# Optimization experiments

Hardware: AMD Instinct MI355X
Metric: run time of the kernel (lower is better)

## Reference

```python
import jax, jax.numpy as jnp
import numpy as np

B, T, LMAX = 8, 4000, 2048
VOCAB, D, H = 20000, 128, 128
SCALE = float(H) ** 0.5  # torch uses pow(hidden_dim, 0.5) with hidden_dim=128 even though feature dim is 256


def setup_inputs() -> dict:
    key = jax.random.key(0)
    ks = jax.random.split(key, 22)
    def n(k, sh, s=0.05):
        return jax.random.normal(k, sh, dtype=jnp.float32) * s
    token_ids = jax.random.randint(ks[0], (B, T), 0, VOCAB)
    lens = jax.random.randint(ks[1], (B,), LMAX // 4, LMAX).at[0].set(LMAX)
    return dict(
        token_ids=token_ids, lens=lens,
        embed=n(ks[2], (VOCAB, D)),
        gru_wih0=n(ks[3], (2, 3 * H, D)), gru_whh0=n(ks[4], (2, 3 * H, H)),
        gru_bih0=n(ks[5], (2, 3 * H)), gru_bhh0=n(ks[6], (2, 3 * H)),
        gru_wih1=n(ks[7], (2, 3 * H, 2 * H)), gru_whh1=n(ks[8], (2, 3 * H, H)),
        gru_bih1=n(ks[9], (2, 3 * H)), gru_bhh1=n(ks[10], (2, 3 * H)),
        conv_w=n(ks[11], (3, D, D, 2)), conv_b=n(ks[12], (3, D)),
        Wa_w=n(ks[13], (2 * H, 4 * H)), Wa_b=n(ks[14], (2 * H,)),
        VT_w=n(ks[15], (1, 2 * H)), VT_b=n(ks[16], (1,)),
        Qw=n(ks[17], (2 * H, 2 * H)), Kw=n(ks[18], (2 * H, 2 * H)), Vw=n(ks[19], (2 * H, 2 * H)),
        fc_w=n(ks[20], (6, 2 * H)), fc_b=n(ks[21], (6,)),
    )


def _gru_dir(x, mask, Wih, Whh, bih, bhh):
    # One direction of a torch GRU layer with packed-sequence semantics:
    # outputs are zero past each sample's length; state frozen there.
    xg = jnp.einsum('bld,gd->blg', x, Wih) + bih   # [B, L, 3H] precomputed input gates
    xg = jnp.swapaxes(xg, 0, 1)                    # [L, B, 3H]
    m = jnp.swapaxes(mask, 0, 1)                   # [L, B]
    h0 = jnp.zeros((x.shape[0], H), x.dtype)

    def step(h, inp):
        g, mt = inp
        hh = h @ Whh.T + bhh
        r = jax.nn.sigmoid(g[:, :H] + hh[:, :H])
        z = jax.nn.sigmoid(g[:, H:2 * H] + hh[:, H:2 * H])
        nn_ = jnp.tanh(g[:, 2 * H:] + r * hh[:, 2 * H:])
        hn = (1.0 - z) * nn_ + z * h
        h2 = jnp.where(mt[:, None] > 0, hn, h)
        return h2, hn * mt[:, None]

    _, out = jax.lax.scan(step, h0, (xg, m))
    return jnp.swapaxes(out, 0, 1)                 # [B, L, H]


def _bi_gru_layer(x, mask, rev_idx, wih, whh, bih, bhh):
    out_f = _gru_dir(x, mask, wih[0], whh[0], bih[0], bhh[0])
    # packed bi-GRU: backward direction runs over each sample's reversed VALID segment
    xr = jnp.take_along_axis(x, rev_idx[:, :, None], axis=1)
    out_b = _gru_dir(xr, mask, wih[1], whh[1], bih[1], bhh[1])
    out_b = jnp.take_along_axis(out_b, rev_idx[:, :, None], axis=1) * mask[:, :, None]
    return jnp.concatenate([out_f, out_b], axis=-1)


def _additive_attn(s, enc, mask, Wa_w, Wa_b, VT_w, VT_b):
    sb = jnp.broadcast_to(s, enc.shape)
    x = jnp.concatenate([sb, enc], axis=-1)                     # [B, L, 4H]
    sh = jnp.tanh(jnp.einsum('blk,hk->blh', x, Wa_w) + Wa_b)
    res = jnp.einsum('blh,oh->blo', sh, VT_w)[..., 0] + VT_b[0]  # [B, L]
    # torch multiplies scores by 0/1 mask BEFORE softmax (pads get score 0, not -inf)
    w = jax.nn.softmax(res * mask, axis=-1)
    return jnp.sum(enc * w[..., None], axis=1, keepdims=True)   # [B, 1, 2H]


def _forward(embed, gru_wih0, gru_whh0, gru_bih0, gru_bhh0, gru_wih1, gru_whh1, gru_bih1, gru_bhh1,
             conv_w, conv_b, Wa_w, Wa_b, VT_w, VT_b, Qw, Kw, Vw, fc_w, fc_b, token_ids, lens):
    emb = embed[token_ids]                                      # [B, T, D]
    tpos = jnp.arange(LMAX)
    mask = (tpos[None, :] < lens[:, None]).astype(emb.dtype)    # [B, LMAX]
    rev_idx = jnp.where(tpos[None, :] < lens[:, None], lens[:, None] - 1 - tpos[None, :], tpos[None, :])
    pad_data = emb[:, :LMAX] * mask[..., None]                  # pad_packed_sequence zeroes pads

    # conv backbone runs on the FULL 4000-length padded embedding (as in torch), then trimmed/masked
    x = jnp.swapaxes(emb, 1, 2)                                 # [B, D, T]
    for i in range(3):
        x = jax.lax.conv_general_dilated(x, conv_w[i], (1,), 'VALID',
                                         dimension_numbers=('NCH', 'OIH', 'NCH'))
        x = jax.nn.relu(x + conv_b[i][None, :, None])
    conv_out = jnp.swapaxes(x, 1, 2)[:, :LMAX] * mask[..., None]  # [B, LMAX, D]

    h1 = _bi_gru_layer(pad_data, mask, rev_idx, gru_wih0, gru_whh0, gru_bih0, gru_bhh0)
    enc = _bi_gru_layer(h1, mask, rev_idx, gru_wih1, gru_whh1, gru_bih1, gru_bhh1)  # [B, LMAX, 2H]

    tmean = jnp.mean(conv_out, axis=1)                          # mean over padded length, as torch
    s = jnp.repeat(tmean, 2, axis=-1)[:, None, :]               # expand+reshape => interleaved duplicate [B,1,2H]

    inp2 = jnp.concatenate([pad_data, pad_data], axis=-1)       # [B, LMAX, 2H]
    Q = inp2 @ Qw.T
    K = inp2 @ Kw.T
    V = inp2 @ Vw.T
    scores = jnp.einsum('bqd,bkd->bqk', Q, K) / SCALE
    W = jax.nn.softmax(scores, axis=0)                          # torch F.softmax implicit dim -> 0 for 3D input
    W = W * mask[:, :, None]                                    # mask broadcast over key axis (query rows masked)
    Z = jnp.einsum('bqk,bkd->bqd', W, V)
    sa = jnp.sum(Z, axis=1, keepdims=True)                      # [B, 1, 2H]

    d1 = _additive_attn(s, enc, mask, Wa_w, Wa_b, VT_w, VT_b)
    d2 = _additive_attn(sa, enc, mask, Wa_w, Wa_b, VT_w, VT_b)
    dinput = 0.5 * (d1 + d2)                                    # mean over the concat dim
    return dinput @ fc_w.T + fc_b                               # [B, 1, 6]


def reference(token_ids, lens, embed, gru_wih0, gru_whh0, gru_bih0, gru_bhh0, gru_wih1, gru_whh1,
              gru_bih1, gru_bhh1, conv_w, conv_b, Wa_w, Wa_b, VT_w, VT_b, Qw, Kw, Vw, fc_w, fc_b):
    return _forward(embed, gru_wih0, gru_whh0, gru_bih0, gru_bhh0, gru_wih1, gru_whh1, gru_bih1,
                    gru_bhh1, conv_w, conv_b, Wa_w, Wa_b, VT_w, VT_b, Qw, Kw, Vw, fc_w, fc_b,
                    token_ids, lens)
```

## Files before the change

kernel.cpp:

```cpp
#include <hip/hip_runtime.h>
#include <stdint.h>

typedef unsigned short u16;
typedef unsigned int u32;
typedef __attribute__((ext_vector_type(8))) short short8;
typedef __attribute__((ext_vector_type(8))) u16 u16x8;
typedef __attribute__((ext_vector_type(4))) float f32x4;
typedef __attribute__((ext_vector_type(2))) float f32x2;
typedef __attribute__((ext_vector_type(2))) u32 u32x2;

#define DEVINL static __device__ __forceinline__

#if !__has_builtin(__builtin_amdgcn_exp2f)
#define __builtin_amdgcn_exp2f(x) exp2f(x)
#endif
#if !__has_builtin(__builtin_amdgcn_rcpf)
#define __builtin_amdgcn_rcpf(x) (1.0f/(x))
#endif

#define MFMA16(a, b, c) __builtin_amdgcn_mfma_f32_16x16x32_bf16((a), (b), (c), 0, 0, 0)

constexpr float LOG2E_C    = 1.4426950408889634f;
constexpr float TWOLOG2E_C = 2.8853900817779268f;
constexpr float RSCALE_LG  = 1.4426950408889634f / 11.313708498984761f;

constexpr size_t A256(size_t x){ return (x + 255) & ~(size_t)255; }
constexpr size_t OFS_EMB   = 0;
constexpr size_t OFS_PAD   = A256(OFS_EMB  + (size_t)8*2051*128*2);
constexpr size_t OFS_X1    = A256(OFS_PAD  + (size_t)8*2048*128*2);
constexpr size_t OFS_X2    = A256(OFS_X1   + (size_t)8*2050*128*2);
constexpr size_t OFS_QKVW  = A256(OFS_X2   + (size_t)8*2049*128*2);
constexpr size_t OFS_WA2   = A256(OFS_QKVW + (size_t)3*256*128*2);
constexpr size_t OFS_CONVW = A256(OFS_WA2  + (size_t)256*256*2);
constexpr size_t OFS_WIH0  = A256(OFS_CONVW+ (size_t)3*128*256*2);
constexpr size_t OFS_WIH1  = A256(OFS_WIH0 + (size_t)2*384*128*2);
constexpr size_t OFS_BIASX = A256(OFS_WIH1 + (size_t)2*384*256*2);
constexpr size_t OFS_BHHN  = A256(OFS_BIASX+ (size_t)2*2*384*4);
constexpr size_t OFS_Q     = A256(OFS_BHHN + (size_t)2*2*128*4);
constexpr size_t OFS_K     = A256(OFS_Q    + (size_t)8*2048*256*2);
constexpr size_t OFS_V     = A256(OFS_K    + (size_t)8*2048*256*2);
constexpr size_t OFS_CS    = A256(OFS_V    + (size_t)8*2048*256*2);
constexpr size_t OFS_TM    = A256(OFS_CS   + (size_t)8*2048*4);
constexpr size_t OFS_XG    = A256(OFS_TM   + (size_t)8*128*4);
constexpr size_t OFS_H1    = A256(OFS_XG   + (size_t)2*2048*8*384*4);
constexpr size_t OFS_ENC   = A256(OFS_H1   + (size_t)8*2048*256*2);
constexpr size_t OFS_ENCW  = A256(OFS_ENC  + (size_t)8*2048*256*2);
constexpr size_t OFS_SA    = A256(OFS_ENCW + (size_t)8*2048*256*4);
constexpr size_t OFS_RES   = A256(OFS_SA   + (size_t)8*256*4);
constexpr size_t OFS_DV    = A256(OFS_RES  + (size_t)8*2*2048*4);

DEVINL u16 f2bf(float f){
  u32 u = __builtin_bit_cast(u32, f);
  u32 r = (u + 0x7FFFu + ((u >> 16) & 1u)) >> 16;
  return (u16)r;
}
DEVINL float bf2f(u16 s){ return __builtin_bit_cast(float, (u32)s << 16); }

DEVINL short8 ld8cvt(const float* p, float sc){
  short8 o;
#pragma unroll
  for (int e = 0; e < 8; ++e) o[e] = (short)f2bf(p[e]*sc);
  return o;
}

DEVINL u32 cvtpk(float lo, float hi){
  u32 r;
  asm("v_cvt_pk_bf16_f32 %0, %1, %2" : "=v"(r) : "v"(lo), "v"(hi));
  return r;
}

DEVINL float sel4(const f32x4 v, int rr){
  float a = (rr & 1) ? v[1] : v[0];
  float bq = (rr & 1) ? v[3] : v[2];
  return (rr & 2) ? bq : a;
}

__global__ __launch_bounds__(256) void k_prep(
    const int* tok, const int* lens, const float* embed,
    const float* wih0, const float* wih1,
    const float* bih0, const float* bhh0, const float* bih1, const float* bhh1,
    const float* convw, const float* WaW, const float* Qw, const float* Kw, const float* Vw,
    char* ws)
{
  u16* emb_bf   = (u16*)(ws + OFS_EMB);
  u16* pad_bf   = (u16*)(ws + OFS_PAD);
  u16* qkvw     = (u16*)(ws + OFS_QKVW);
  u16* wa2      = (u16*)(ws + OFS_WA2);
  u16* convw_bf = (u16*)(ws + OFS_CONVW);
  u16* wih0_bf  = (u16*)(ws + OFS_WIH0);
  u16* wih1_bf  = (u16*)(ws + OFS_WIH1);
  float* biasx  = (float*)(ws + OFS_BIASX);
  float* bhhn   = (float*)(ws + OFS_BHHN);
  float* colsum = (float*)(ws + OFS_CS);
  float* tmean  = (float*)(ws + OFS_TM);
  const int S0 = 8*2051*128, S1 = 8*2048*128, S2 = 3*256*128, S3 = 256*256, S4 = 3*128*256;
  const int S5 = 2*384*128, S6 = 2*384*256, S7 = 2*2*384 + 2*2*128, S8 = 8*2048 + 8*128;
  const int TOT = S0+S1+S2+S3+S4+S5+S6+S7+S8;
  for (int i = blockIdx.x*256 + threadIdx.x; i < TOT; i += gridDim.x*256){
    int j = i;
    if (j < S0){
      int b = j / (2051*128); int r = j - b*(2051*128); int t = r >> 7, dd = r & 127;
      emb_bf[j] = f2bf(embed[(size_t)tok[b*4000 + t]*128 + dd]);
      continue;
    }
    j -= S0;
    if (j < S1){
      int b = j >> 18; int r = j & 262143; int t = r >> 7, dd = r & 127;
      float v = (t < lens[b]) ? embed[(size_t)tok[b*4000 + t]*128 + dd] : 0.f;
      pad_bf[j] = f2bf(v); continue;
    }
    j -= S1;
    if (j < S2){
      int z = j >> 15; int r = j & 32767; int o = r >> 7, k2 = r & 127;
      const float* W = (z == 0) ? Qw : (z == 1) ? Kw : Vw;
      qkvw[j] = f2bf(W[o*256 + k2] + W[o*256 + 128 + k2]); continue;
    }
    j -= S2;
    if (j < S3){ int h = j >> 8, k2 = j & 255; wa2[j] = f2bf(WaW[(size_t)h*512 + 256 + k2]); continue; }
    j -= S3;
    if (j < S4){
      int ly = j >> 15; int r = j & 32767; int o = r >> 8, k2 = r & 255;
      int i2 = k2 & 127, kap = k2 >> 7;
      convw_bf[j] = f2bf(convw[((size_t)(ly*128 + o)*128 + i2)*2 + kap]); continue;
    }
    j -= S4;
    if (j < S5){ wih0_bf[j] = f2bf(wih0[j]); continue; }
    j -= S5;
    if (j < S6){ wih1_bf[j] = f2bf(wih1[j]); continue; }
    j -= S6;
    if (j < S7){
      if (j < 1536){
        int ly = j / 768; int r = j - ly*768; int d = r / 384, g = r % 384;
        float bi = (ly ? bih1 : bih0)[d*384 + g];
        float bh = (ly ? bhh1 : bhh0)[d*384 + g];
        biasx[j] = (g < 256) ? (-LOG2E_C*(bi + bh)) : (TWOLOG2E_C*bi);
      } else {
        int j2 = j - 1536; int ly = j2 >> 8; int r = j2 & 255; int d = r >> 7, jj = r & 127;
        bhhn[j2] = TWOLOG2E_C*((ly ? bhh1 : bhh0)[d*384 + 256 + jj]);
      }
      continue;
    }
    j -= S7;
    if (j < 8*2048) colsum[j] = 0.f; else tmean[j - 8*2048] = 0.f;
  }
}

template<int KIN>
__global__ __launch_bounds__(256, 1) void k_xg(const int* lens, char* ws){
  const int tt = blockIdx.x, b = blockIdx.y, dir = blockIdx.z;
  constexpr int LAYER = (KIN == 128) ? 0 : 1;
  const u16* in = (KIN == 128) ? (const u16*)(ws + OFS_PAD) : (const u16*)(ws + OFS_H1);
  const u16* wmat = ((KIN == 128) ? (const u16*)(ws + OFS_WIH0) : (const u16*)(ws + OFS_WIH1))
                    + (size_t)dir*384*KIN;
  const float* biasx = (const float*)(ws + OFS_BIASX) + (LAYER*2 + dir)*384;
  float* xg = (float*)(ws + OFS_XG) + (size_t)dir*2048*3072;
  const int lenb = lens[b];
  __shared__ __align__(16) u16 sA[64][KIN + 8];
  constexpr int CH = KIN/8;
  const int tid = threadIdx.x, w = tid >> 6, l = tid & 63, rowg = l >> 4, cl = l & 15;
  for (int idx = tid; idx < 64*CH; idx += 256){
    int row = idx / CH, chn = idx % CH;
    int t = tt*64 + row;
    int tr = dir ? ((t < lenb) ? (lenb - 1 - t) : t) : t;
    *(u16x8*)&sA[row][chn*8] = *(const u16x8*)(in + ((size_t)(b*2048 + tr))*KIN + chn*8);
  }
  __syncthreads();
  f32x4 acc[24];
#pragma unroll
  for (int nt = 0; nt < 24; ++nt) acc[nt] = f32x4{0.f,0.f,0.f,0.f};
#pragma unroll
  for (int kk = 0; kk < KIN/32; ++kk){
    short8 a = *(const short8*)&sA[w*16 + cl][kk*32 + rowg*8];
#pragma unroll
    for (int nt = 0; nt < 24; ++nt){
      short8 bb = *(const short8*)(wmat + (size_t)(nt*16 + cl)*KIN + kk*32 + rowg*8);
      acc[nt] = MFMA16(a, bb, acc[nt]);
    }
  }
#pragma unroll
  for (int nt = 0; nt < 24; ++nt){
    const int g = nt*16 + cl;
    const float bx = biasx[g];
    const float sc = (nt < 16) ? -LOG2E_C : TWOLOG2E_C;
#pragma unroll
    for (int r = 0; r < 4; ++r){
      const int t = tt*64 + w*16 + rowg*4 + r;
      xg[((size_t)t*8 + b)*384 + g] = sc*acc[nt][r] + bx;
    }
  }
}

DEVINL void rec_block(char* smem, const float* xg_all, const float* whh_all,
    const float* bhhn_all, const int* lens, u16* out, int dir, int b)
{
  const float* xg  = xg_all + (size_t)dir*2048*3072 + b*384;
  const float* whh = whh_all + (size_t)dir*384*128;
  const float* bnd = bhhn_all + dir*128;
  const int tid = threadIdx.x;
  const int u = tid >> 6, l = tid & 63;
  const int c = l & 15, q = l >> 4;
  const int rsel = c & 3;
  const int j = u*16 + q*4 + rsel;
  const bool writer = (c < 4);
  const bool dirb = (dir != 0);
  const int lenb = lens[b];

  u16 (*hbuf)[128] = (u16(*)[128])smem;
  if (tid < 256) (&hbuf[0][0])[tid] = 0;

  short8 aR[4], aZ[4], aN[4];
#pragma unroll
  for (int kk = 0; kk < 4; ++kk){
    int k0 = kk*32 + q*8;
    int row = u*16 + c;
    aR[kk] = ld8cvt(whh + (size_t)(row)*128 + k0, -LOG2E_C);
    aZ[kk] = ld8cvt(whh + (size_t)(128 + row)*128 + k0, -LOG2E_C);
    aN[kk] = ld8cvt(whh + (size_t)(256 + row)*128 + k0, TWOLOG2E_C);
  }
  f32x4 bnU;
#pragma unroll
  for (int r = 0; r < 4; ++r) bnU[r] = bnd[u*16 + q*4 + r];

  const int offR = u*16 + q*4;
  const int offXN = 256 + j;
  u16* outp = out + (size_t)b*2048*256 + dir*128 + j;
  float hp = 0.f;

#define LOAD_STAGE(T_, Rv, Zv, Xn) do {              \
    const float* pb_ = xg + (size_t)(T_)*3072;       \
    Rv = *(const f32x4*)(pb_ + offR);                \
    Zv = *(const f32x4*)(pb_ + offR + 128);          \
    Xn = pb_[offXN];                                 \
  } while (0)

#define REC_STEP(T_, PF_, CUR_, Rv, Zv, Xn) do {                                      \
    short8 bf0_ = *(const short8*)(&hbuf[CUR_][0] + (q*8 + 0*32));                    \
    short8 bf1_ = *(const short8*)(&hbuf[CUR_][0] + (q*8 + 1*32));                    \
    short8 bf2_ = *(const short8*)(&hbuf[CUR_][0] + (q*8 + 2*32));                    \
    short8 bf3_ = *(const short8*)(&hbuf[CUR_][0] + (q*8 + 3*32));                    \
    f32x4 cR_ = MFMA16(aR[0], bf0_, Rv);                                              \
    f32x4 cZ_ = MFMA16(aZ[0], bf0_, Zv);                                              \
    f32x4 cN_ = MFMA16(aN[0], bf0_, bnU);                                             \
    const float* pfb_ = xg + (size_t)(PF_)*3072;                                      \
    Rv = *(const f32x4*)(pfb_ + offR);                                                \
    Zv = *(const f32x4*)(pfb_ + offR + 128);                                          \
    float Xnew_ = pfb_[offXN];                                                        \
    cR_ = MFMA16(aR[1], bf1_, cR_);                                                   \
    cZ_ = MFMA16(aZ[1], bf1_, cZ_);                                                   \
    cN_ = MFMA16(aN[1], bf1_, cN_);                                                   \
    cR_ = MFMA16(aR[2], bf2_, cR_);                                                   \
    cZ_ = MFMA16(aZ[2], bf2_, cZ_);                                                   \
    cN_ = MFMA16(aN[2], bf2_, cN_);                                                   \
    cR_ = MFMA16(aR[3], bf3_, cR_);                                                   \
    cZ_ = MFMA16(aZ[3], bf3_, cZ_);                                                   \
    cN_ = MFMA16(aN[3], bf3_, cN_);                                                   \
    const bool v_ = (T_) < lenb;                                                      \
    float gR = sel4(cR_, rsel);                                                       \
    float gZ = sel4(cZ_, rsel);                                                       \
    float gN = sel4(cN_, rsel);                                                       \
    float Rg = __builtin_amdgcn_rcpf(1.f + __builtin_amdgcn_exp2f(gR));               \
    float Zg = __builtin_amdgcn_rcpf(1.f + __builtin_amdgcn_exp2f(gZ));               \
    float y  = Xn + Rg*gN;                                                            \
    float NN = 1.f - 2.f*__builtin_amdgcn_rcpf(1.f + __builtin_amdgcn_exp2f(y));      \
    float hn = NN + Zg*(hp - NN);                                                     \
    hp = hn;                                                                          \
    Xn = Xnew_;                                                                       \
    u32 pk_ = cvtpk(hn, hn);                                                          \
    if (writer){                                                                      \
      hbuf[(CUR_) ^ 1][j] = (u16)pk_;                                                 \
      int to_ = dirb ? (v_ ? (lenb - 1 - (T_)) : (T_)) : (T_);                        \
      outp[(size_t)to_*256] = v_ ? (u16)pk_ : (u16)0;                                 \
    }                                                                                 \
    asm volatile("s_waitcnt lgkmcnt(0)" ::: "memory");                                \
    __builtin_amdgcn_s_barrier();                                                     \
  } while (0)

  f32x4 R0v, Z0v; float X0;
  f32x4 R1v, Z1v; float X1;
  f32x4 R2v, Z2v; float X2;
  f32x4 R3v, Z3v; float X3;
  __syncthreads();
  LOAD_STAGE(0, R0v, Z0v, X0);
  LOAD_STAGE(1, R1v, Z1v, X1);
  LOAD_STAGE(2, R2v, Z2v, X2);
  LOAD_STAGE(3, R3v, Z3v, X3);
  for (int t = 0; t < 2048; t += 4){
    int p4 = (t + 4 < 2048) ? (t + 4) : 2047;
    int p5 = (t + 5 < 2048) ? (t + 5) : 2047;
    int p6 = (t + 6 < 2048) ? (t + 6) : 2047;
    int p7 = (t + 7 < 2048) ? (t + 7) : 2047;
    REC_STEP(t + 0, p4, 0, R0v, Z0v, X0);
    REC_STEP(t + 1, p5, 1, R1v, Z1v, X1);
    REC_STEP(t + 2, p6, 0, R2v, Z2v, X2);
    REC_STEP(t + 3, p7, 1, R3v, Z3v, X3);
  }
#undef LOAD_STAGE
#undef REC_STEP
}

DEVINL void qkv_role(char* smem, char* ws, int tt, int b, int z){
  const u16* in = (const u16*)(ws + OFS_PAD);
  const u16* wmat = (const u16*)(ws + OFS_QKVW) + (size_t)z*256*128;
  u16* out = (u16*)(ws + ((z == 0) ? OFS_Q : (z == 1) ? OFS_K : OFS_V));
  u16 (*sA)[136] = (u16(*)[136])smem;
  const int tid = threadIdx.x;
  if (tid < 256){
    for (int idx = tid; idx < 64*16; idx += 256){
      int row = idx >> 4, chn = idx & 15;
      int t = tt*64 + row;
      *(u16x8*)&sA[row][chn*8] = *(const u16x8*)(in + ((size_t)(b*2048 + t))*128 + chn*8);
    }
  }
  __syncthreads();
  if (tid < 256){
    const int w = tid >> 6, l = tid & 63, rowg = l >> 4, cl = l & 15;
    f32x4 acc[16];
#pragma unroll
    for (int nt = 0; nt < 16; ++nt) acc[nt] = f32x4{0.f,0.f,0.f,0.f};
#pragma unroll
    for (int kk = 0; kk < 4; ++kk){
      short8 a = *(const short8*)&sA[w*16 + cl][kk*32 + rowg*8];
#pragma unroll
      for (int nt = 0; nt < 16; ++nt){
        short8 bb = *(const short8*)(wmat + (size_t)(nt*16 + cl)*128 + kk*32 + rowg*8);
        acc[nt] = MFMA16(a, bb, acc[nt]);
      }
    }
#pragma unroll
    for (int nt = 0; nt < 16; ++nt){
      int o = nt*16 + cl;
#pragma unroll
      for (int r = 0; r < 4; ++r){
        int t = tt*64 + w*16 + rowg*4 + r;
        out[((size_t)(b*2048 + t))*256 + o] = f2bf(acc[nt][r]);
      }
    }
  }
}

DEVINL void conv_layer_pass(u16 (*bi)[136], u16 (*bo)[136], const u16* wm, const float* bias,
                            int OUT_R, int w, int rowg, int cl){
#pragma unroll
  for (int pass = 0; pass < 2; ++pass){
    if (pass == 1 && !(w == 0 && OUT_R > 64)) break;
    const int rt = (pass == 0) ? w : 4;
    f32x4 acc[8];
#pragma unroll
    for (int nt = 0; nt < 8; ++nt) acc[nt] = f32x4{0.f,0.f,0.f,0.f};
#pragma unroll
    for (int kk = 0; kk < 8; ++kk){
      const int rofs = (kk >= 4) ? 1 : 0;
      short8 a = *(const short8*)&bi[rt*16 + cl + rofs][(kk & 3)*32 + rowg*8];
#pragma unroll
      for (int nt = 0; nt < 8; ++nt){
        short8 bb = *(const short8*)(wm + (size_t)(nt*16 + cl)*256 + kk*32 + rowg*8);
        acc[nt] = MFMA16(a, bb, acc[nt]);
      }
    }
#pragma unroll
    for (int nt = 0; nt < 8; ++nt){
      int o = nt*16 + cl;
      float bv = bias[o];
#pragma unroll
      for (int r = 0; r < 4; ++r){
        int ro = rt*16 + rowg*4 + r;
        if (ro < OUT_R) bo[ro][o] = f2bf(fmaxf(acc[nt][r] + bv, 0.f));
      }
    }
  }
}

DEVINL void conv_role(char* smem, const int* lens, const float* convb, char* ws, int tt, int b){
  const u16* emb = (const u16*)(ws + OFS_EMB);
  const u16* cw  = (const u16*)(ws + OFS_CONVW);
  float* tmean = (float*)(ws + OFS_TM);
  u16 (*bufA)[136] = (u16(*)[136])smem;
  u16 (*bufB)[136] = (u16(*)[136])(smem + 82*136*2);
  const int tid = threadIdx.x;
  const int w = tid >> 6, l = tid & 63, rowg = l >> 4, cl = l & 15;
  if (tid < 256){
    for (int idx = tid; idx < 67*16; idx += 256){
      int row = idx >> 4, chn = idx & 15;
      *(u16x8*)&bufA[row][chn*8] = *(const u16x8*)(emb + ((size_t)(b*2051 + tt*64 + row))*128 + chn*8);
    }
  }
  __syncthreads();
  if (tid < 256) conv_layer_pass(bufA, bufB, cw + (size_t)0*128*256, convb + 0,   66, w, rowg, cl);
  __syncthreads();
  if (tid < 256) conv_layer_pass(bufB, bufA, cw + (size_t)1*128*256, convb + 128, 65, w, rowg, cl);
  __syncthreads();
  if (tid < 256){
    const int lenb = lens[b];
    const u16* wm = cw + (size_t)2*128*256;
    f32x4 acc[8];
#pragma unroll
    for (int nt = 0; nt < 8; ++nt) acc[nt] = f32x4{0.f,0.f,0.f,0.f};
#pragma unroll
    for (int kk = 0; kk < 8; ++kk){
      const int rofs = (kk >= 4) ? 1 : 0;
      short8 a = *(const short8*)&bufA[w*16 + cl + rofs][(kk & 3)*32 + rowg*8];
#pragma unroll
      for (int nt = 0; nt < 8; ++nt){
        short8 bb = *(const short8*)(wm + (size_t)(nt*16 + cl)*256 + kk*32 + rowg*8);
        acc[nt] = MFMA16(a, bb, acc[nt]);
      }
    }
#pragma unroll
    for (int nt = 0; nt < 8; ++nt){
      int o = nt*16 + cl;
      float bias = convb[2*128 + o];
      float s = 0.f;
#pragma unroll
      for (int r = 0; r < 4; ++r){
        int t = tt*64 + w*16 + rowg*4 + r;
        if (t < lenb) s += fmaxf(acc[nt][r] + bias, 0.f);
      }
      s += __shfl_xor(s, 16); s += __shfl_xor(s, 32);
      if (l < 16) atomicAdd(&tmean[b*128 + o], s);
    }
  }
}

DEVINL void scores_role(char* smem, const int* lens, char* ws, int kt, int qt){
  const u16* Qp = (const u16*)(ws + OFS_Q);
  const u16* Kp = (const u16*)(ws + OFS_K);
  float* colsum = (float*)(ws + OFS_CS);
  u16 (*sQ)[264] = (u16(*)[264])smem;
  u16 (*sK)[264] = (u16(*)[264])(smem + 64*264*2);
  float (*cbuf)[64] = (float(*)[64])(smem + 2*64*264*2);
  const int tid = threadIdx.x, w = tid >> 6, l = tid & 63, rowg = l >> 4, cl = l & 15;
  if (tid < 256)
    for (int i = tid; i < 512; i += 256) cbuf[i >> 6][i & 63] = 0.f;
  f32x4 c[8][4];
#pragma unroll
  for (int b = 0; b < 8; ++b)
#pragma unroll
    for (int nt = 0; nt < 4; ++nt) c[b][nt] = f32x4{0.f,0.f,0.f,0.f};
#pragma unroll
  for (int b = 0; b < 8; ++b){
    __syncthreads();
    if (tid < 256){
      for (int idx = tid; idx < 4096; idx += 256){
        int which = idx >> 11, row = (idx >> 5) & 63, ch = idx & 31;
        if (which){
          *(u16x8*)&sK[row][ch*8] = *(const u16x8*)(Kp + ((size_t)(b*2048 + kt*64 + row))*256 + ch*8);
        } else {
          *(u16x8*)&sQ[row][ch*8] = *(const u16x8*)(Qp + ((size_t)(b*2048 + qt*64 + row))*256 + ch*8);
        }
      }
    }
    __syncthreads();
    if (tid < 256){
#pragma unroll
      for (int kk = 0; kk < 8; ++kk){
        short8 a = *(const short8*)&sQ[w*16 + cl][kk*32 + rowg*8];
#pragma unroll
        for (int nt = 0; nt < 4; ++nt){
          short8 bb = *(const short8*)&sK[nt*16 + cl][kk*32 + rowg*8];
          c[b][nt] = MFMA16(a, bb, c[b][nt]);
        }
      }
    }
  }
  if (tid < 256){
    int lenv[8];
#pragma unroll
    for (int b = 0; b < 8; ++b) lenv[b] = lens[b];
    const int q0 = qt*64 + w*16 + rowg*4;
    float cs[8][4];
#pragma unroll
    for (int b = 0; b < 8; ++b)
#pragma unroll
      for (int nt = 0; nt < 4; ++nt) cs[b][nt] = 0.f;
#pragma unroll
    for (int nt = 0; nt < 4; ++nt){
#pragma unroll
      for (int r = 0; r < 4; ++r){
        float m = c[0][nt][r];
#pragma unroll
        for (int b = 1; b < 8; ++b) m = fmaxf(m, c[b][nt][r]);
        float e[8], s = 0.f;
#pragma unroll
        for (int b = 0; b < 8; ++b){ e[b] = __builtin_amdgcn_exp2f((c[b][nt][r] - m)*RSCALE_LG); s += e[b]; }
        float ri = __builtin_amdgcn_rcpf(s);
#pragma unroll
        for (int b = 0; b < 8; ++b)
          if (q0 + r < lenv[b]) cs[b][nt] += e[b]*ri;
      }
    }
#pragma unroll
    for (int b = 0; b < 8; ++b)
#pragma unroll
      for (int nt = 0; nt < 4; ++nt){
        float v = cs[b][nt];
        v += __shfl_xor(v, 16); v += __shfl_xor(v, 32);
        if (l < 16) atomicAdd(&cbuf[b][nt*16 + l], v);
      }
  }
  __syncthreads();
  if (tid < 256){
    for (int i = tid; i < 512; i += 256)
      atomicAdd(&colsum[(size_t)(i >> 6)*2048 + kt*64 + (i & 63)], cbuf[i >> 6][i & 63]);
  }
}

__global__ __launch_bounds__(512, 2) void k_fusedA(const int* lens, const float* convb, char* ws,
    const float* whh0, u16* outH1)
{
  __shared__ __align__(16) char smem[90112];
  const int bid = blockIdx.x;
  if (bid < 16){
    rec_block(smem, (const float*)(ws + OFS_XG), whh0, (const float*)(ws + OFS_BHHN),
              lens, outH1, bid >> 3, bid & 7);
    return;
  }
  int r = bid - 16;
  if (r < 768){
    int z = r >> 8, rem = r & 255, b = rem >> 5, tt = rem & 31;
    qkv_role(smem, ws, tt, b, z);
    return;
  }
  r -= 768;
  conv_role(smem, lens, convb, ws, r & 31, r >> 5);
}

__global__ __launch_bounds__(512, 2) void k_fusedB(const int* lens, char* ws,
    const float* whh1, u16* outENC)
{
  __shared__ __align__(16) char smem[90112];
  const int bid = blockIdx.x;
  if (bid < 16){
    rec_block(smem, (const float*)(ws + OFS_XG), whh1, (const float*)(ws + OFS_BHHN) + 2*128,
              lens, outENC, bid >> 3, bid & 7);
    return;
  }
  int r = bid - 16;
  scores_role(smem, lens, ws, r & 31, r >> 5);
}

__global__ __launch_bounds__(256, 1) void k_encw(char* ws){
  const int tt = blockIdx.x, b = blockIdx.y;
  const u16* in = (const u16*)(ws + OFS_ENC);
  const u16* wmat = (const u16*)(ws + OFS_WA2);
  float* out = (float*)(ws + OFS_ENCW);
  __shared__ __align__(16) u16 sA[64][264];
  const int tid = threadIdx.x, w = tid >> 6, l = tid & 63, rowg = l >> 4, cl = l & 15;
  for (int idx = tid; idx < 64*32; idx += 256){
    int row = idx >> 5, chn = idx & 31;
    int t = tt*64 + row;
    *(u16x8*)&sA[row][chn*8] = *(const u16x8*)(in + ((size_t)(b*2048 + t))*256 + chn*8);
  }
  __syncthreads();
  f32x4 acc[16];
#pragma unroll
  for (int nt = 0; nt < 16; ++nt) acc[nt] = f32x4{0.f,0.f,0.f,0.f};
#pragma unroll
  for (int kk = 0; kk < 8; ++kk){
    short8 a = *(const short8*)&sA[w*16 + cl][kk*32 + rowg*8];
#pragma unroll
    for (int nt = 0; nt < 16; ++nt){
      short8 bb = *(const short8*)(wmat + (size_t)(nt*16 + cl)*256 + kk*32 + rowg*8);
      acc[nt] = MFMA16(a, bb, acc[nt]);
    }
  }
#pragma unroll
  for (int nt = 0; nt < 16; ++nt){
    int h = nt*16 + cl;
#pragma unroll
    for (int r = 0; r < 4; ++r){
      int t = tt*64 + w*16 + rowg*4 + r;
      out[((size_t)(b*2048 + t))*256 + h] = acc[nt][r];
    }
  }
}

__global__ __launch_bounds__(256) void k_sa(char* ws){
  const int b = blockIdx.x, d = threadIdx.x;
  const float* cs = (const float*)(ws + OFS_CS) + (size_t)b*2048;
  const u16* V = (const u16*)(ws + OFS_V) + (size_t)b*2048*256;
  float a0 = 0.f, a1 = 0.f, a2 = 0.f, a3 = 0.f;
  for (int k = 0; k < 2048; k += 4){
    a0 += cs[k + 0]*bf2f(V[(size_t)(k + 0)*256 + d]);
    a1 += cs[k + 1]*bf2f(V[(size_t)(k + 1)*256 + d]);
    a2 += cs[k + 2]*bf2f(V[(size_t)(k + 2)*256 + d]);
    a3 += cs[k + 3]*bf2f(V[(size_t)(k + 3)*256 + d]);
  }
  ((float*)(ws + OFS_SA))[b*256 + d] = (a0 + a1) + (a2 + a3);
}

__global__ __launch_bounds__(256) void k_res(const int* lens, const float* WaW, const float* Wab,
    const float* VTw, const float* VTb, char* ws){
  const int b = blockIdx.x, x = blockIdx.y, chb = blockIdx.z;
  const float* tm = (const float*)(ws + OFS_TM) + b*128;
  const float* sa = (const float*)(ws + OFS_SA) + b*256;
  const float* encW = (const float*)(ws + OFS_ENCW);
  float* res = (float*)(ws + OFS_RES) + ((size_t)b*2 + x)*2048;
  __shared__ float sw[256];
  __shared__ float vt[256];
  const int tid = threadIdx.x;
  {
    int h = tid;
    float acc = Wab[h];
    if (x == 0){
      for (int j = 0; j < 128; ++j)
        acc += tm[j]*(1.f/2048.f)*(WaW[(size_t)h*512 + 2*j] + WaW[(size_t)h*512 + 2*j + 1]);
    } else {
      for (int k = 0; k < 256; ++k) acc += sa[k]*WaW[(size_t)h*512 + k];
    }
    sw[h] = acc;
    vt[h] = VTw[h];
  }
  __syncthreads();
  const int lenb = lens[b];
  const int lsub = tid >> 2, q = tid & 3;
  const float vtb = VTb[0];
#pragma unroll
  for (int pass = 0; pass < 4; ++pass){
    const int ll = chb*256 + pass*64 + lsub;
    const float* er = encW + ((size_t)(b*2048 + ll))*256 + q*64;
    float racc = 0.f;
    for (int j = 0; j < 64; ++j){
      float u = er[j] + sw[q*64 + j];
      float th = 1.f - 2.f*__builtin_amdgcn_rcpf(1.f + __builtin_amdgcn_exp2f(u*TWOLOG2E_C));
      racc += th*vt[q*64 + j];
    }
    racc += __shfl_xor(racc, 1);
    racc += __shfl_xor(racc, 2);
    if (q == 0) res[ll] = (ll < lenb) ? (racc + vtb) : 0.f;
  }
}

__global__ __launch_bounds__(256) void k_attnfin(char* ws){
  const int b = blockIdx.x, x = blockIdx.y;
  const float* res = (const float*)(ws + OFS_RES) + ((size_t)b*2 + x)*2048;
  const u16* enc = (const u16*)(ws + OFS_ENC);
  float* dvec = (float*)(ws + OFS_DV);
  __shared__ float sv[2048];
  __shared__ float red[8];
  const int tid = threadIdx.x;
  float m = -3.0e38f;
  for (int i = tid; i < 2048; i += 256){ float v = res[i]; sv[i] = v; m = fmaxf(m, v); }
#pragma unroll
  for (int o = 1; o < 64; o <<= 1) m = fmaxf(m, __shfl_xor(m, o));
  if ((tid & 63) == 0) red[tid >> 6] = m;
  __syncthreads();
  m = fmaxf(fmaxf(red[0], red[1]), fmaxf(red[2], red[3]));
  __syncthreads();
  float s = 0.f;
  for (int i = tid; i < 2048; i += 256){ float e = __builtin_amdgcn_exp2f((sv[i] - m)*LOG2E_C); sv[i] = e; s += e; }
#pragma unroll
  for (int o = 1; o < 64; o <<= 1) s += __shfl_xor(s, o);
  if ((tid & 63) == 0) red[tid >> 6] = s;
  __syncthreads();
  const float S = red[0] + red[1] + red[2] + red[3];
  const float ri = 1.0f/S;
  const int h = tid;
  float a0 = 0.f, a1 = 0.f, a2 = 0.f, a3 = 0.f;
  for (int l0 = 0; l0 < 2048; l0 += 4){
    a0 += sv[l0 + 0]*bf2f(enc[((size_t)(b*2048 + l0 + 0))*256 + h]);
    a1 += sv[l0 + 1]*bf2f(enc[((size_t)(b*2048 + l0 + 1))*256 + h]);
    a2 += sv[l0 + 2]*bf2f(enc[((size_t)(b*2048 + l0 + 2))*256 + h]);
    a3 += sv[l0 + 3]*bf2f(enc[((size_t)(b*2048 + l0 + 3))*256 + h]);
  }
  dvec[((size_t)b*2 + x)*256 + h] = ((a0 + a1) + (a2 + a3))*ri;
}

__global__ __launch_bounds__(64) void k_final(const float* fcw, const float* fcb, char* ws, float* outp){
  const int i = threadIdx.x;
  if (i >= 48) return;
  const int b = i/6, o = i%6;
  const float* dv = (const float*)(ws + OFS_DV);
  float acc = fcb[o];
  for (int h = 0; h < 256; ++h)
    acc += 0.5f*(dv[((size_t)b*2 + 0)*256 + h] + dv[((size_t)b*2 + 1)*256 + h])*fcw[o*256 + h];
  outp[i] = acc;
}

extern "C" void kernel_launch(void* const* d_in, const int* in_sizes, int n_in,
                              void* d_out, int out_size, void* d_ws, size_t ws_size,
                              hipStream_t stream)
{
  const int* tok    = (const int*)d_in[0];
  const int* lens   = (const int*)d_in[1];
  const float* embed= (const float*)d_in[2];
  const float* wih0 = (const float*)d_in[3];
  const float* whh0 = (const float*)d_in[4];
  const float* bih0 = (const float*)d_in[5];
  const float* bhh0 = (const float*)d_in[6];
  const float* wih1 = (const float*)d_in[7];
  const float* whh1 = (const float*)d_in[8];
  const float* bih1 = (const float*)d_in[9];
  const float* bhh1 = (const float*)d_in[10];
  const float* convw= (const float*)d_in[11];
  const float* convb= (const float*)d_in[12];
  const float* WaW  = (const float*)d_in[13];
  const float* Wab  = (const float*)d_in[14];
  const float* VTw  = (const float*)d_in[15];
  const float* VTb  = (const float*)d_in[16];
  const float* Qw   = (const float*)d_in[17];
  const float* Kw   = (const float*)d_in[18];
  const float* Vw   = (const float*)d_in[19];
  const float* fcw  = (const float*)d_in[20];
  const float* fcb  = (const float*)d_in[21];
  char* ws = (char*)d_ws;
  float* outp = (float*)d_out;

  hipLaunchKernelGGL(k_prep, dim3(2048), dim3(256), 0, stream,
      tok, lens, embed, wih0, wih1, bih0, bhh0, bih1, bhh1, convw, WaW, Qw, Kw, Vw, ws);
  hipLaunchKernelGGL((k_xg<128>), dim3(32,8,2), dim3(256), 0, stream, lens, ws);
  hipLaunchKernelGGL(k_fusedA, dim3(16 + 768 + 256), dim3(512), 0, stream,
      lens, convb, ws, whh0, (u16*)(ws + OFS_H1));
  hipLaunchKernelGGL((k_xg<256>), dim3(32,8,2), dim3(256), 0, stream, lens, ws);
  hipLaunchKernelGGL(k_fusedB, dim3(16 + 1024), dim3(512), 0, stream,
      lens, ws, whh1, (u16*)(ws + OFS_ENC));
  hipLaunchKernelGGL(k_sa, dim3(8), dim3(256), 0, stream, ws);
  hipLaunchKernelGGL(k_encw, dim3(32,8), dim3(256), 0, stream, ws);
  hipLaunchKernelGGL(k_res, dim3(8,2,8), dim3(256), 0, stream, lens, WaW, Wab, VTw, VTb, ws);
  hipLaunchKernelGGL(k_attnfin, dim3(8,2), dim3(256), 0, stream, ws);
  hipLaunchKernelGGL(k_final, dim3(1), dim3(64), 0, stream, fcw, fcb, ws, outp);
  (void)in_sizes; (void)n_in; (void)out_size; (void)ws_size;
}
```

Measured before the change: 1.799 ms.

## Merge tail kernels, split attention reduction, raise MFMA priority in recurrence

Merges k_encw and k_sa into a single launch (k_tail1) that branches on block index. It also splits k_attnfin's 2048-step reduction across 4 z-blocks that combine partial sums with atomicAdd into a dvec buffer now zeroed in k_prep. The GRU recurrence wraps its MFMA chain in s_setprio(1)/s_setprio(0) to favor the latency-critical wave. The aim is to cut launch overhead and serial tail latency; the cost is redundant softmax work per chunk and non-deterministic float accumulation order.

```diff
diff --git a/kernel.cpp b/kernel.cpp
--- a/kernel.cpp
+++ b/kernel.cpp
@@ -93,8 +93,10 @@
   float* bhhn   = (float*)(ws + OFS_BHHN);
   float* colsum = (float*)(ws + OFS_CS);
   float* tmean  = (float*)(ws + OFS_TM);
+  float* dvec   = (float*)(ws + OFS_DV);
   const int S0 = 8*2051*128, S1 = 8*2048*128, S2 = 3*256*128, S3 = 256*256, S4 = 3*128*256;
-  const int S5 = 2*384*128, S6 = 2*384*256, S7 = 2*2*384 + 2*2*128, S8 = 8*2048 + 8*128;
+  const int S5 = 2*384*128, S6 = 2*384*256, S7 = 2*2*384 + 2*2*128;
+  const int S8 = 8*2048 + 8*128 + 8*2*256;
   const int TOT = S0+S1+S2+S3+S4+S5+S6+S7+S8;
   for (int i = blockIdx.x*256 + threadIdx.x; i < TOT; i += gridDim.x*256){
     int j = i;
@@ -141,7 +143,10 @@
       continue;
     }
     j -= S7;
-    if (j < 8*2048) colsum[j] = 0.f; else tmean[j - 8*2048] = 0.f;
+    if (j < 8*2048){ colsum[j] = 0.f; continue; }
+    j -= 8*2048;
+    if (j < 8*128){ tmean[j] = 0.f; continue; }
+    dvec[j - 8*128] = 0.f;
   }
 }
 
@@ -238,6 +243,7 @@
     short8 bf1_ = *(const short8*)(&hbuf[CUR_][0] + (q*8 + 1*32));                    \
     short8 bf2_ = *(const short8*)(&hbuf[CUR_][0] + (q*8 + 2*32));                    \
     short8 bf3_ = *(const short8*)(&hbuf[CUR_][0] + (q*8 + 3*32));                    \
+    __builtin_amdgcn_s_setprio(1);                                                    \
     f32x4 cR_ = MFMA16(aR[0], bf0_, Rv);                                              \
     f32x4 cZ_ = MFMA16(aZ[0], bf0_, Zv);                                              \
     f32x4 cN_ = MFMA16(aN[0], bf0_, bnU);                                             \
@@ -254,6 +260,7 @@
     cR_ = MFMA16(aR[3], bf3_, cR_);                                                   \
     cZ_ = MFMA16(aZ[3], bf3_, cZ_);                                                   \
     cN_ = MFMA16(aN[3], bf3_, cN_);                                                   \
+    __builtin_amdgcn_s_setprio(0);                                                    \
     const bool v_ = (T_) < lenb;                                                      \
     float gR = sel4(cR_, rsel);                                                       \
     float gZ = sel4(cZ_, rsel);                                                       \
@@ -538,54 +545,55 @@
   scores_role(smem, lens, ws, r & 31, r >> 5);
 }
 
-__global__ __launch_bounds__(256, 1) void k_encw(char* ws){
-  const int tt = blockIdx.x, b = blockIdx.y;
-  const u16* in = (const u16*)(ws + OFS_ENC);
-  const u16* wmat = (const u16*)(ws + OFS_WA2);
-  float* out = (float*)(ws + OFS_ENCW);
+__global__ __launch_bounds__(256, 1) void k_tail1(char* ws){
   __shared__ __align__(16) u16 sA[64][264];
-  const int tid = threadIdx.x, w = tid >> 6, l = tid & 63, rowg = l >> 4, cl = l & 15;
-  for (int idx = tid; idx < 64*32; idx += 256){
-    int row = idx >> 5, chn = idx & 31;
-    int t = tt*64 + row;
-    *(u16x8*)&sA[row][chn*8] = *(const u16x8*)(in + ((size_t)(b*2048 + t))*256 + chn*8);
-  }
-  __syncthreads();
-  f32x4 acc[16];
-#pragma unroll
-  for (int nt = 0; nt < 16; ++nt) acc[nt] = f32x4{0.f,0.f,0.f,0.f};
-#pragma unroll
-  for (int kk = 0; kk < 8; ++kk){
-    short8 a = *(const short8*)&sA[w*16 + cl][kk*32 + rowg*8];
+  const int bid = blockIdx.x;
+  if (bid < 256){
+    const int tt = bid & 31, b = bid >> 5;
+    const u16* in = (const u16*)(ws + OFS_ENC);
+    const u16* wmat = (const u16*)(ws + OFS_WA2);
+    float* out = (float*)(ws + OFS_ENCW);
+    const int tid = threadIdx.x, w = tid >> 6, l = tid & 63, rowg = l >> 4, cl = l & 15;
+    for (int idx = tid; idx < 64*32; idx += 256){
+      int row = idx >> 5, chn = idx & 31;
+      int t = tt*64 + row;
+      *(u16x8*)&sA[row][chn*8] = *(const u16x8*)(in + ((size_t)(b*2048 + t))*256 + chn*8);
+    }
+    __syncthreads();
+    f32x4 acc[16];
+#pragma unroll
+    for (int nt = 0; nt < 16; ++nt) acc[nt] = f32x4{0.f,0.f,0.f,0.f};
+#pragma unroll
+    for (int kk = 0; kk < 8; ++kk){
+      short8 a = *(const short8*)&sA[w*16 + cl][kk*32 + rowg*8];
+#pragma unroll
+      for (int nt = 0; nt < 16; ++nt){
+        short8 bb = *(const short8*)(wmat + (size_t)(nt*16 + cl)*256 + kk*32 + rowg*8);
+        acc[nt] = MFMA16(a, bb, acc[nt]);
+      }
+    }
 #pragma unroll
     for (int nt = 0; nt < 16; ++nt){
-      short8 bb = *(const short8*)(wmat + (size_t)(nt*16 + cl)*256 + kk*32 + rowg*8);
-      acc[nt] = MFMA16(a, bb, acc[nt]);
-    }
-  }
-#pragma unroll
-  for (int nt = 0; nt < 16; ++nt){
-    int h = nt*16 + cl;
-#pragma unroll
-    for (int r = 0; r < 4; ++r){
-      int t = tt*64 + w*16 + rowg*4 + r;
-      out[((size_t)(b*2048 + t))*256 + h] = acc[nt][r];
-    }
-  }
-}
-
-__global__ __launch_bounds__(256) void k_sa(char* ws){
-  const int b = blockIdx.x, d = threadIdx.x;
-  const float* cs = (const float*)(ws + OFS_CS) + (size_t)b*2048;
-  const u16* V = (const u16*)(ws + OFS_V) + (size_t)b*2048*256;
-  float a0 = 0.f, a1 = 0.f, a2 = 0.f, a3 = 0.f;
-  for (int k = 0; k < 2048; k += 4){
-    a0 += cs[k + 0]*bf2f(V[(size_t)(k + 0)*256 + d]);
-    a1 += cs[k + 1]*bf2f(V[(size_t)(k + 1)*256 + d]);
-    a2 += cs[k + 2]*bf2f(V[(size_t)(k + 2)*256 + d]);
-    a3 += cs[k + 3]*bf2f(V[(size_t)(k + 3)*256 + d]);
-  }
-  ((float*)(ws + OFS_SA))[b*256 + d] = (a0 + a1) + (a2 + a3);
+      int h = nt*16 + cl;
+#pragma unroll
+      for (int r = 0; r < 4; ++r){
+        int t = tt*64 + w*16 + rowg*4 + r;
+        out[((size_t)(b*2048 + t))*256 + h] = acc[nt][r];
+      }
+    }
+  } else {
+    const int b = bid - 256, d = threadIdx.x;
+    const float* cs = (const float*)(ws + OFS_CS) + (size_t)b*2048;
+    const u16* V = (const u16*)(ws + OFS_V) + (size_t)b*2048*256;
+    float a0 = 0.f, a1 = 0.f, a2 = 0.f, a3 = 0.f;
+    for (int k = 0; k < 2048; k += 4){
+      a0 += cs[k + 0]*bf2f(V[(size_t)(k + 0)*256 + d]);
+      a1 += cs[k + 1]*bf2f(V[(size_t)(k + 1)*256 + d]);
+      a2 += cs[k + 2]*bf2f(V[(size_t)(k + 2)*256 + d]);
+      a3 += cs[k + 3]*bf2f(V[(size_t)(k + 3)*256 + d]);
+    }
+    ((float*)(ws + OFS_SA))[b*256 + d] = (a0 + a1) + (a2 + a3);
+  }
 }
 
 __global__ __launch_bounds__(256) void k_res(const int* lens, const float* WaW, const float* Wab,
@@ -631,7 +639,7 @@
 }
 
 __global__ __launch_bounds__(256) void k_attnfin(char* ws){
-  const int b = blockIdx.x, x = blockIdx.y;
+  const int b = blockIdx.x, x = blockIdx.y, ch = blockIdx.z;
   const float* res = (const float*)(ws + OFS_RES) + ((size_t)b*2 + x)*2048;
   const u16* enc = (const u16*)(ws + OFS_ENC);
   float* dvec = (float*)(ws + OFS_DV);
@@ -655,14 +663,15 @@
   const float S = red[0] + red[1] + red[2] + red[3];
   const float ri = 1.0f/S;
   const int h = tid;
+  const int l0b = ch*512;
   float a0 = 0.f, a1 = 0.f, a2 = 0.f, a3 = 0.f;
-  for (int l0 = 0; l0 < 2048; l0 += 4){
+  for (int l0 = l0b; l0 < l0b + 512; l0 += 4){
     a0 += sv[l0 + 0]*bf2f(enc[((size_t)(b*2048 + l0 + 0))*256 + h]);
     a1 += sv[l0 + 1]*bf2f(enc[((size_t)(b*2048 + l0 + 1))*256 + h]);
     a2 += sv[l0 + 2]*bf2f(enc[((size_t)(b*2048 + l0 + 2))*256 + h]);
     a3 += sv[l0 + 3]*bf2f(enc[((size_t)(b*2048 + l0 + 3))*256 + h]);
   }
-  dvec[((size_t)b*2 + x)*256 + h] = ((a0 + a1) + (a2 + a3))*ri;
+  atomicAdd(&dvec[((size_t)b*2 + x)*256 + h], ((a0 + a1) + (a2 + a3))*ri);
 }
 
 __global__ __launch_bounds__(64) void k_final(const float* fcw, const float* fcb, char* ws, float* outp){
@@ -713,10 +722,9 @@
   hipLaunchKernelGGL((k_xg<256>), dim3(32,8,2), dim3(256), 0, stream, lens, ws);
   hipLaunchKernelGGL(k_fusedB, dim3(16 + 1024), dim3(512), 0, stream,
       lens, ws, whh1, (u16*)(ws + OFS_ENC));
-  hipLaunchKernelGGL(k_sa, dim3(8), dim3(256), 0, stream, ws);
-  hipLaunchKernelGGL(k_encw, dim3(32,8), dim3(256), 0, stream, ws);
+  hipLaunchKernelGGL(k_tail1, dim3(264), dim3(256), 0, stream, ws);
   hipLaunchKernelGGL(k_res, dim3(8,2,8), dim3(256), 0, stream, lens, WaW, Wab, VTw, VTb, ws);
-  hipLaunchKernelGGL(k_attnfin, dim3(8,2), dim3(256), 0, stream, ws);
+  hipLaunchKernelGGL(k_attnfin, dim3(8,2,4), dim3(256), 0, stream, ws);
   hipLaunchKernelGGL(k_final, dim3(1), dim3(64), 0, stream, fcw, fcb, ws, outp);
   (void)in_sizes; (void)n_in; (void)out_size; (void)ws_size;
 }
```

Measured after the change: 1.739 ms. 1.03x faster.
